# Kernel optimization log

Hardware: AMD Instinct MI355X
Metric: run time of the kernel (lower is better)

## Reference

```python
import jax, jax.numpy as jnp
import numpy as np

EPS = 1e-5  # torch BatchNorm default


def setup_inputs() -> dict:
    key = jax.random.key(0)
    ks = jax.random.split(key, 8)
    B, Q, S, C = 4, 256, 128, 256
    feats = [2 * C, 256, 64, 1]  # opt['num_features']
    inp = {
        "support_features": jax.random.normal(ks[0], (B, S, C), dtype=jnp.float32),
        "query_features": jax.random.normal(ks[1], (B, Q, C), dtype=jnp.float32),
    }
    for i in range(3):
        fan_in, fan_out = feats[i], feats[i + 1]
        std = np.sqrt(2.0 / (fan_in + fan_out))  # xavier_normal on conv weight
        inp[f"W{i}"] = jax.random.normal(ks[2 + i], (fan_out, fan_in), dtype=jnp.float32) * std
        inp[f"b{i}"] = jnp.zeros((fan_out,), dtype=jnp.float32)
        inp[f"g{i}"] = jnp.ones((fan_out,), dtype=jnp.float32)   # BN weight
        inp[f"bt{i}"] = jnp.zeros((fan_out,), dtype=jnp.float32)  # BN bias
    return inp


def _bn_relu(x, g, bt):
    # x: [B, N, C]; BatchNorm1d training-mode stats over batch and length dims
    mean = jnp.mean(x, axis=(0, 1))
    var = jnp.mean(jnp.square(x - mean), axis=(0, 1))  # biased var, as torch BN
    return jax.nn.relu((x - mean) * (g * jax.lax.rsqrt(var + EPS)) + bt)


def reference(support_features, query_features,
              W0, b0, g0, bt0, W1, b1, g1, bt1, W2, b2, g2, bt2):
    B, S, C = support_features.shape
    Q = query_features.shape[1]
    # pairwise concat: [B, Q, S, 2C]
    uq = jnp.broadcast_to(query_features[:, :, None, :], (B, Q, S, C))
    us = jnp.broadcast_to(support_features[:, None, :, :], (B, Q, S, C))
    x = jnp.concatenate([uq, us], axis=3).reshape(B, Q * S, 2 * C)
    # 1x1 conv == matmul over channel dim
    x = _bn_relu(jnp.einsum('bnc,oc->bno', x, W0) + b0, g0, bt0)
    x = _bn_relu(jnp.einsum('bnc,oc->bno', x, W1) + b1, g1, bt1)
    x = _bn_relu(jnp.einsum('bnc,oc->bno', x, W2) + b2, g2, bt2)
    # back to [B, C_out, Q, S]
    return jnp.transpose(x, (0, 2, 1)).reshape(B, -1, Q, S)
```

## Files before the change

### kernel.cpp

```cpp
#include <hip/hip_runtime.h>
#include <hip/hip_bf16.h>


typedef __attribute__((ext_vector_type(4))) float f32x4;
typedef __attribute__((ext_vector_type(8))) short s16x8;

#define BN_EPS 1e-5f
#define INV_N  (1.0f/131072.0f)
#define W1PITCH 264

__device__ __forceinline__ unsigned pk_bf16(float a, float b) {
  float2 t; t.x = a; t.y = b;
  __hip_bfloat162 h = __float22bfloat162_rn(t);
  return *reinterpret_cast<unsigned*>(&h);
}
__device__ __forceinline__ void split2(float a, float b, unsigned& uh, unsigned& ul) {
  uh = pk_bf16(a, b);
  float ha = __uint_as_float(uh << 16);
  float hb = __uint_as_float(uh & 0xFFFF0000u);
  ul = pk_bf16(a - ha, b - hb);
}

union frag_u { s16x8 v; unsigned u[4]; };

struct Args {
  const float *Sf, *Qf, *W0, *b0, *g0, *bt0, *W1, *b1, *g1, *bt1, *W2, *b2, *g2, *bt2;
  float *Aq, *As, *y2, *ws0s, *ws1f, *ws2f, *out;
  ushort *W1h, *W1l;
};

__global__ __launch_bounds__(256) void k_g0(Args a)
{
  int bi = blockIdx.x, t = threadIdx.x;
  if (bi == 96) {
    for (int k = 0; k < 32; k++) {
      int idx = t * 64 + k * 2;
      unsigned uh, ul;
      split2(a.W1[idx], a.W1[idx + 1], uh, ul);
      a.W1h[idx] = (ushort)(uh & 0xFFFFu); a.W1h[idx + 1] = (ushort)(uh >> 16);
      a.W1l[idx] = (ushort)(ul & 0xFFFFu); a.W1l[idx + 1] = (ushort)(ul >> 16);
    }
    for (int i = t; i < 2048; i += 256) a.ws1f[i] = 0.0f;
    if (t < 32) a.ws2f[t] = 0.0f;
    return;
  }
  int w = t >> 6, l = t & 63, l15 = l & 15, quad = l >> 4;
  bool isQ = (bi < 64);
  const float* X; float* Out; int m0, koff;
  if (isQ) { m0 = bi * 16; X = a.Qf; Out = a.Aq; koff = 0; }
  else     { m0 = (bi - 64) * 16; X = a.Sf; Out = a.As; koff = 256; }
  int n0 = w * 64;

  f32x4 acc[4] = {};
#pragma unroll
  for (int ko = 0; ko < 256; ko += 32) {
    const float* row = X + (m0 + l15) * 256 + ko + quad * 8;
    f32x4 v0 = *(const f32x4*)(row);
    f32x4 v1 = *(const f32x4*)(row + 4);
    frag_u ah, al;
#pragma unroll
    for (int j = 0; j < 2; j++) {
      split2(v0[2 * j], v0[2 * j + 1], ah.u[j], al.u[j]);
      split2(v1[2 * j], v1[2 * j + 1], ah.u[2 + j], al.u[2 + j]);
    }
#pragma unroll
    for (int nt = 0; nt < 4; nt++) {
      const float* wrow = a.W0 + (n0 + nt * 16 + l15) * 512 + koff + ko + quad * 8;
      f32x4 w0v = *(const f32x4*)(wrow);
      f32x4 w1v = *(const f32x4*)(wrow + 4);
      frag_u bh, bl;
      split2(w0v[0], w0v[1], bh.u[0], bl.u[0]);
      split2(w0v[2], w0v[3], bh.u[1], bl.u[1]);
      split2(w1v[0], w1v[1], bh.u[2], bl.u[2]);
      split2(w1v[2], w1v[3], bh.u[3], bl.u[3]);
      acc[nt] = __builtin_amdgcn_mfma_f32_16x16x32_bf16(ah.v, bh.v, acc[nt], 0, 0, 0);
      acc[nt] = __builtin_amdgcn_mfma_f32_16x16x32_bf16(al.v, bh.v, acc[nt], 0, 0, 0);
      acc[nt] = __builtin_amdgcn_mfma_f32_16x16x32_bf16(ah.v, bl.v, acc[nt], 0, 0, 0);
    }
  }
#pragma unroll
  for (int nt = 0; nt < 4; nt++) {
    int o = n0 + nt * 16 + l15;
    float bias = isQ ? 0.0f : a.b0[o];
    float cs = 0, cs2 = 0;
#pragma unroll
    for (int r = 0; r < 4; r++) {
      float y = acc[nt][r] + bias;
      Out[(m0 + quad * 4 + r) * 256 + o] = y;
      cs += y; cs2 += y * y;
    }
    cs  += __shfl_xor(cs, 16);  cs  += __shfl_xor(cs, 32);
    cs2 += __shfl_xor(cs2, 16); cs2 += __shfl_xor(cs2, 32);
    if (quad == 0) {
      a.ws0s[bi * 512 + o] = cs;
      a.ws0s[bi * 512 + 256 + o] = cs2;
    }
  }
}

__device__ __forceinline__ void stage_w1(const Args& a, int t, ushort* w1h, ushort* w1l)
{
  int row = t >> 2, qd = t & 3;
  const s16x8* srch = (const s16x8*)(a.W1h + row * 256 + qd * 64);
  const s16x8* srcl = (const s16x8*)(a.W1l + row * 256 + qd * 64);
  s16x8* dsth = (s16x8*)(w1h + row * W1PITCH + qd * 64);
  s16x8* dstl = (s16x8*)(w1l + row * W1PITCH + qd * 64);
#pragma unroll
  for (int k = 0; k < 8; k++) { dsth[k] = srch[k]; dstl[k] = srcl[k]; }
}

__device__ __forceinline__ void mfma_kloop(
    const float* __restrict__ Aq, const float* __restrict__ As,
    const float* sh_a0c0, const ushort* w1h, const ushort* w1l,
    int b, int qt, int st, int w, int l15, int quad, f32x4 acc[4][4])
{
  const float* asrow = As + ((b << 7) + st * 16 + l15) * 256;
  const float* aqrow[4];
#pragma unroll
  for (int mt = 0; mt < 4; mt++)
    aqrow[mt] = Aq + ((b << 8) + qt * 16 + w * 4 + mt) * 256;

#pragma unroll
  for (int ko = 0; ko < 256; ko += 32) {
    int obase = ko + quad * 8;
    f32x4 a0v0 = *(const f32x4*)(sh_a0c0 + obase);
    f32x4 a0v1 = *(const f32x4*)(sh_a0c0 + obase + 4);
    f32x4 c0v0 = *(const f32x4*)(sh_a0c0 + 256 + obase);
    f32x4 c0v1 = *(const f32x4*)(sh_a0c0 + 256 + obase + 4);
    f32x4 as0 = *(const f32x4*)(asrow + obase);
    f32x4 as1 = *(const f32x4*)(asrow + obase + 4);

    s16x8 zh[4];
#pragma unroll
    for (int mt = 0; mt < 4; mt++) {
      f32x4 aq0 = *(const f32x4*)(aqrow[mt] + obase);
      f32x4 aq1 = *(const f32x4*)(aqrow[mt] + obase + 4);
      f32x4 z0 = (aq0 + as0) * a0v0 + c0v0;
      f32x4 z1 = (aq1 + as1) * a0v1 + c0v1;
      frag_u zz;
      zz.u[0] = pk_bf16(fmaxf(z0[0], 0.0f), fmaxf(z0[1], 0.0f));
      zz.u[1] = pk_bf16(fmaxf(z0[2], 0.0f), fmaxf(z0[3], 0.0f));
      zz.u[2] = pk_bf16(fmaxf(z1[0], 0.0f), fmaxf(z1[1], 0.0f));
      zz.u[3] = pk_bf16(fmaxf(z1[2], 0.0f), fmaxf(z1[3], 0.0f));
      zh[mt] = zz.v;
    }
#pragma unroll
    for (int nt = 0; nt < 4; nt++) {
      s16x8 bh = *(const s16x8*)(w1h + (nt * 16 + l15) * W1PITCH + obase);
      s16x8 bl = *(const s16x8*)(w1l + (nt * 16 + l15) * W1PITCH + obase);
#pragma unroll
      for (int mt = 0; mt < 4; mt++) {
        acc[mt][nt] = __builtin_amdgcn_mfma_f32_16x16x32_bf16(zh[mt], bh, acc[mt][nt], 0, 0, 0);
        acc[mt][nt] = __builtin_amdgcn_mfma_f32_16x16x32_bf16(zh[mt], bl, acc[mt][nt], 0, 0, 0);
      }
    }
  }
}

__device__ __forceinline__ void bn0_finalize(const Args& a, int t, float* sh_a0c0)
{
  int o = t;
  float sumY = 0, cross = 0, SQ2 = 0, SS2 = 0;
#pragma unroll
  for (int b = 0; b < 4; b++) {
    float sq1 = 0, sq2 = 0, ss1 = 0, ss2 = 0;
#pragma unroll
    for (int c = 0; c < 16; c++) {
      sq1 += a.ws0s[(b * 16 + c) * 512 + o];
      sq2 += a.ws0s[(b * 16 + c) * 512 + 256 + o];
    }
#pragma unroll
    for (int c = 0; c < 8; c++) {
      ss1 += a.ws0s[(64 + b * 8 + c) * 512 + o];
      ss2 += a.ws0s[(64 + b * 8 + c) * 512 + 256 + o];
    }
    SQ2 += sq2; SS2 += ss2;
    sumY += 128.0f * sq1 + 256.0f * ss1;
    cross += sq1 * ss1;
  }
  float mean = sumY * INV_N;
  float var = (128.0f * SQ2 + 256.0f * SS2 + 2.0f * cross) * INV_N - mean * mean;
  float aa = a.g0[o] * rsqrtf(var + BN_EPS);
  sh_a0c0[o] = aa;
  sh_a0c0[256 + o] = a.bt0[o] - mean * aa;
}

__global__ __launch_bounds__(256) void k_m1(Args a)
{
  int bi = blockIdx.x, t = threadIdx.x;
  int w = t >> 6, l = t & 63, l15 = l & 15, quad = l >> 4;
  __shared__ ushort w1h[64 * W1PITCH];
  __shared__ ushort w1l[64 * W1PITCH];
  __shared__ float sh_a0c0[512];
  __shared__ float red[2][4][4][16];

  stage_w1(a, t, w1h, w1l);
  bn0_finalize(a, t, sh_a0c0);
  __syncthreads();

  int b_ = bi >> 7, rem = bi & 127, qt = rem >> 3, st = rem & 7;
  f32x4 acc[4][4] = {};
  mfma_kloop(a.Aq, a.As, sh_a0c0, w1h, w1l, b_, qt, st, w, l15, quad, acc);

#pragma unroll
  for (int nt = 0; nt < 4; nt++) {
    float bias = a.b1[nt * 16 + l15];
    float s = 0, s2 = 0;
#pragma unroll
    for (int mt = 0; mt < 4; mt++)
#pragma unroll
      for (int r = 0; r < 4; r++) {
        float y = acc[mt][nt][r] + bias;
        s += y; s2 += y * y;
      }
    s  += __shfl_xor(s, 16);  s  += __shfl_xor(s, 32);
    s2 += __shfl_xor(s2, 16); s2 += __shfl_xor(s2, 32);
    if (quad == 0) { red[0][w][nt][l15] = s; red[1][w][nt][l15] = s2; }
  }
  __syncthreads();
  if (t < 128) {
    int which = t >> 6, j = t & 63, nt = j >> 4, jl = j & 15;
    float v = red[which][0][nt][jl] + red[which][1][nt][jl] +
              red[which][2][nt][jl] + red[which][3][nt][jl];
    atomicAdd(&a.ws1f[(bi & 15) * 128 + t], v);
  }
}

__global__ __launch_bounds__(256) void k_m2(Args a)
{
  int bi = blockIdx.x, t = threadIdx.x;
  int w = t >> 6, l = t & 63, l15 = l & 15, quad = l >> 4;
  __shared__ ushort w1h[64 * W1PITCH];
  __shared__ ushort w1l[64 * W1PITCH];
  __shared__ float sh_a0c0[512];
  __shared__ float sh_tot[128];
  __shared__ float sh_a1c1[128];
  __shared__ float rs[16], rs2[16];

  stage_w1(a, t, w1h, w1l);
  bn0_finalize(a, t, sh_a0c0);
  if (t < 128) {
    float accv = 0;
#pragma unroll
    for (int c = 0; c < 16; c++) accv += a.ws1f[c * 128 + t];
    sh_tot[t] = accv;
  }
  __syncthreads();
  if (t < 64) {
    float mean = sh_tot[t] * INV_N;
    float var = sh_tot[64 + t] * INV_N - mean * mean;
    float aa = a.g1[t] * rsqrtf(var + BN_EPS);
    sh_a1c1[t] = aa;
    sh_a1c1[64 + t] = a.bt1[t] - mean * aa;
  }
  __syncthreads();

  int b_ = bi >> 7, rem = bi & 127, qt = rem >> 3, st = rem & 7;
  f32x4 acc[4][4] = {};
  mfma_kloop(a.Aq, a.As, sh_a0c0, w1h, w1l, b_, qt, st, w, l15, quad, acc);

  float a1v[4], c1v[4], w2v[4], biasv[4];
#pragma unroll
  for (int nt = 0; nt < 4; nt++) {
    int j = nt * 16 + l15;
    a1v[nt] = sh_a1c1[j]; c1v[nt] = sh_a1c1[64 + j];
    w2v[nt] = a.W2[j]; biasv[nt] = a.b1[j];
  }
  float b2v = a.b2[0];
  float ls = 0, ls2 = 0;
#pragma unroll
  for (int mt = 0; mt < 4; mt++) {
    float part[4] = {0, 0, 0, 0};
#pragma unroll
    for (int nt = 0; nt < 4; nt++)
#pragma unroll
      for (int r = 0; r < 4; r++) {
        float y = acc[mt][nt][r] + biasv[nt];
        float z = fmaxf(a1v[nt] * y + c1v[nt], 0.0f);
        part[r] += z * w2v[nt];
      }
#pragma unroll
    for (int r = 0; r < 4; r++) {
      float p = part[r];
      p += __shfl_xor(p, 1); p += __shfl_xor(p, 2);
      p += __shfl_xor(p, 4); p += __shfl_xor(p, 8);
      part[r] = p + b2v;
    }
    if (l15 == 0) {
      int q = qt * 16 + w * 4 + mt;
      int P = ((b_ * 256 + q) * 128) + st * 16 + quad * 4;
      f32x4 o;
#pragma unroll
      for (int r = 0; r < 4; r++) { o[r] = part[r]; ls += part[r]; ls2 += part[r] * part[r]; }
      *(f32x4*)(a.y2 + P) = o;
    }
  }
  if (l15 == 0) { rs[t >> 4] = ls; rs2[t >> 4] = ls2; }
  __syncthreads();
  if (t == 0) {
    float s = 0, s2 = 0;
#pragma unroll
    for (int i = 0; i < 16; i++) { s += rs[i]; s2 += rs2[i]; }
    atomicAdd(&a.ws2f[(bi & 15) * 2], s);
    atomicAdd(&a.ws2f[(bi & 15) * 2 + 1], s2);
  }
}

__global__ __launch_bounds__(256) void k_out(Args a)
{
  int t = threadIdx.x;
  float s = 0, s2 = 0;
#pragma unroll
  for (int c = 0; c < 16; c++) { s += a.ws2f[c * 2]; s2 += a.ws2f[c * 2 + 1]; }
  float mean = s * INV_N;
  float var = s2 * INV_N - mean * mean;
  float aa = a.g2[0] * rsqrtf(var + BN_EPS);
  float cc = a.bt2[0] - mean * aa;
  int i = (blockIdx.x * 256 + t) * 4;
  f32x4 v = *(const f32x4*)(a.y2 + i);
  f32x4 o;
#pragma unroll
  for (int r = 0; r < 4; r++) o[r] = fmaxf(aa * v[r] + cc, 0.0f);
  *(f32x4*)(a.out + i) = o;
}

extern "C" void kernel_launch(void* const* d_in, const int* in_sizes, int n_in,
                              void* d_out, int out_size, void* d_ws, size_t ws_size,
                              hipStream_t stream)
{
  float* ws = (float*)d_ws;
  Args a;
  a.Sf  = (const float*)d_in[0];
  a.Qf  = (const float*)d_in[1];
  a.W0  = (const float*)d_in[2];
  a.b0  = (const float*)d_in[3];
  a.g0  = (const float*)d_in[4];
  a.bt0 = (const float*)d_in[5];
  a.W1  = (const float*)d_in[6];
  a.b1  = (const float*)d_in[7];
  a.g1  = (const float*)d_in[8];
  a.bt1 = (const float*)d_in[9];
  a.W2  = (const float*)d_in[10];
  a.b2  = (const float*)d_in[11];
  a.g2  = (const float*)d_in[12];
  a.bt2 = (const float*)d_in[13];

  a.Aq   = ws;
  a.As   = ws + 262144;
  a.y2   = ws + 393216;
  a.ws0s = ws + 524288;
  a.ws1f = ws + 573440;
  a.ws2f = ws + 575488;
  a.W1h  = (ushort*)(ws + 575552);
  a.W1l  = (ushort*)(ws + 583744);
  a.out  = (float*)d_out;

  k_g0 <<<97, 256, 0, stream>>>(a);
  k_m1 <<<512, 256, 0, stream>>>(a);
  k_m2 <<<512, 256, 0, stream>>>(a);
  k_out<<<128, 256, 0, stream>>>(a);
}
```

Baseline: 144.2 us.

## Materialize layer-1 output in bf16 instead of recomputing GEMM in second pass

```diff
diff --git a/kernel.cpp b/kernel.cpp
--- a/kernel.cpp
+++ b/kernel.cpp
@@ -7,7 +7,6 @@
 
 #define BN_EPS 1e-5f
 #define INV_N  (1.0f/131072.0f)
-#define W1PITCH 264
 
 __device__ __forceinline__ unsigned pk_bf16(float a, float b) {
   float2 t; t.x = a; t.y = b;
@@ -26,7 +25,7 @@
 struct Args {
   const float *Sf, *Qf, *W0, *b0, *g0, *bt0, *W1, *b1, *g1, *bt1, *W2, *b2, *g2, *bt2;
   float *Aq, *As, *y2, *ws0s, *ws1f, *ws2f, *out;
-  ushort *W1h, *W1l;
+  ushort *W1h, *W1l, *y1f;
 };
 
 __global__ __launch_bounds__(256) void k_g0(Args a)
@@ -98,31 +97,65 @@
   }
 }
 
-__device__ __forceinline__ void stage_w1(const Args& a, int t, ushort* w1h, ushort* w1l)
-{
-  int row = t >> 2, qd = t & 3;
-  const s16x8* srch = (const s16x8*)(a.W1h + row * 256 + qd * 64);
-  const s16x8* srcl = (const s16x8*)(a.W1l + row * 256 + qd * 64);
-  s16x8* dsth = (s16x8*)(w1h + row * W1PITCH + qd * 64);
-  s16x8* dstl = (s16x8*)(w1l + row * W1PITCH + qd * 64);
-#pragma unroll
-  for (int k = 0; k < 8; k++) { dsth[k] = srch[k]; dstl[k] = srcl[k]; }
-}
-
-__device__ __forceinline__ void mfma_kloop(
-    const float* __restrict__ Aq, const float* __restrict__ As,
-    const float* sh_a0c0, const ushort* w1h, const ushort* w1l,
-    int b, int qt, int st, int w, int l15, int quad, f32x4 acc[4][4])
-{
-  const float* asrow = As + ((b << 7) + st * 16 + l15) * 256;
+__device__ __forceinline__ void bn0_finalize(const Args& a, int t, float* sh_a0c0)
+{
+  int o = t;
+  float sumY = 0, cross = 0, SQ2 = 0, SS2 = 0;
+#pragma unroll
+  for (int b = 0; b < 4; b++) {
+    float sq1 = 0, sq2 = 0, ss1 = 0, ss2 = 0;
+#pragma unroll
+    for (int c = 0; c < 16; c++) {
+      sq1 += a.ws0s[(b * 16 + c) * 512 + o];
+      sq2 += a.ws0s[(b * 16 + c) * 512 + 256 + o];
+    }
+#pragma unroll
+    for (int c = 0; c < 8; c++) {
+      ss1 += a.ws0s[(64 + b * 8 + c) * 512 + o];
+      ss2 += a.ws0s[(64 + b * 8 + c) * 512 + 256 + o];
+    }
+    SQ2 += sq2; SS2 += ss2;
+    sumY += 128.0f * sq1 + 256.0f * ss1;
+    cross += sq1 * ss1;
+  }
+  float mean = sumY * INV_N;
+  float var = (128.0f * SQ2 + 256.0f * SS2 + 2.0f * cross) * INV_N - mean * mean;
+  float aa = a.g0[o] * rsqrtf(var + BN_EPS);
+  sh_a0c0[o] = aa;
+  sh_a0c0[256 + o] = a.bt0[o] - mean * aa;
+}
+
+__global__ __launch_bounds__(256) void k_m1(Args a)
+{
+  int bi = blockIdx.x, t = threadIdx.x;
+  int w = t >> 6, l = t & 63, l15 = l & 15, quad = l >> 4;
+  __shared__ ushort w1hf[2048 * 8];
+  __shared__ ushort w1lf[2048 * 8];
+  __shared__ float sh_a0c0[512];
+  __shared__ float red[2][4][4][16];
+
+#pragma unroll
+  for (int i = 0; i < 8; i++) {
+    int fr = i * 256 + t;
+    int kk = fr >> 8, r = fr & 255, nt = r >> 6, ln = r & 63;
+    int src = (nt * 16 + (ln & 15)) * 256 + kk * 32 + (ln >> 4) * 8;
+    *(s16x8*)(w1hf + fr * 8) = *(const s16x8*)(a.W1h + src);
+    *(s16x8*)(w1lf + fr * 8) = *(const s16x8*)(a.W1l + src);
+  }
+  bn0_finalize(a, t, sh_a0c0);
+  __syncthreads();
+
+  int b_ = bi >> 7, rem = bi & 127, qt = rem >> 3, st = rem & 7;
+  const float* asrow = a.As + ((b_ << 7) + st * 16 + l15) * 256;
   const float* aqrow[4];
 #pragma unroll
   for (int mt = 0; mt < 4; mt++)
-    aqrow[mt] = Aq + ((b << 8) + qt * 16 + w * 4 + mt) * 256;
-
-#pragma unroll
-  for (int ko = 0; ko < 256; ko += 32) {
-    int obase = ko + quad * 8;
+    aqrow[mt] = a.Aq + ((b_ << 8) + qt * 16 + w * 4 + mt) * 256;
+
+  f32x4 acc[4][4] = {};
+#pragma unroll
+  for (int kk = 0; kk < 8; kk++) {
+    int obase = kk * 32 + quad * 8;
     f32x4 a0v0 = *(const f32x4*)(sh_a0c0 + obase);
     f32x4 a0v1 = *(const f32x4*)(sh_a0c0 + obase + 4);
     f32x4 c0v0 = *(const f32x4*)(sh_a0c0 + 256 + obase);
@@ -146,8 +179,8 @@
     }
 #pragma unroll
     for (int nt = 0; nt < 4; nt++) {
-      s16x8 bh = *(const s16x8*)(w1h + (nt * 16 + l15) * W1PITCH + obase);
-      s16x8 bl = *(const s16x8*)(w1l + (nt * 16 + l15) * W1PITCH + obase);
+      s16x8 bh = *(const s16x8*)(w1hf + ((kk * 4 + nt) * 64 + l) * 8);
+      s16x8 bl = *(const s16x8*)(w1lf + ((kk * 4 + nt) * 64 + l) * 8);
 #pragma unroll
       for (int mt = 0; mt < 4; mt++) {
         acc[mt][nt] = __builtin_amdgcn_mfma_f32_16x16x32_bf16(zh[mt], bh, acc[mt][nt], 0, 0, 0);
@@ -155,67 +188,35 @@
       }
     }
   }
-}
-
-__device__ __forceinline__ void bn0_finalize(const Args& a, int t, float* sh_a0c0)
-{
-  int o = t;
-  float sumY = 0, cross = 0, SQ2 = 0, SS2 = 0;
-#pragma unroll
-  for (int b = 0; b < 4; b++) {
-    float sq1 = 0, sq2 = 0, ss1 = 0, ss2 = 0;
-#pragma unroll
-    for (int c = 0; c < 16; c++) {
-      sq1 += a.ws0s[(b * 16 + c) * 512 + o];
-      sq2 += a.ws0s[(b * 16 + c) * 512 + 256 + o];
-    }
-#pragma unroll
-    for (int c = 0; c < 8; c++) {
-      ss1 += a.ws0s[(64 + b * 8 + c) * 512 + o];
-      ss2 += a.ws0s[(64 + b * 8 + c) * 512 + 256 + o];
-    }
-    SQ2 += sq2; SS2 += ss2;
-    sumY += 128.0f * sq1 + 256.0f * ss1;
-    cross += sq1 * ss1;
-  }
-  float mean = sumY * INV_N;
-  float var = (128.0f * SQ2 + 256.0f * SS2 + 2.0f * cross) * INV_N - mean * mean;
-  float aa = a.g0[o] * rsqrtf(var + BN_EPS);
-  sh_a0c0[o] = aa;
-  sh_a0c0[256 + o] = a.bt0[o] - mean * aa;
-}
-
-__global__ __launch_bounds__(256) void k_m1(Args a)
-{
-  int bi = blockIdx.x, t = threadIdx.x;
-  int w = t >> 6, l = t & 63, l15 = l & 15, quad = l >> 4;
-  __shared__ ushort w1h[64 * W1PITCH];
-  __shared__ ushort w1l[64 * W1PITCH];
-  __shared__ float sh_a0c0[512];
-  __shared__ float red[2][4][4][16];
-
-  stage_w1(a, t, w1h, w1l);
-  bn0_finalize(a, t, sh_a0c0);
-  __syncthreads();
-
-  int b_ = bi >> 7, rem = bi & 127, qt = rem >> 3, st = rem & 7;
-  f32x4 acc[4][4] = {};
-  mfma_kloop(a.Aq, a.As, sh_a0c0, w1h, w1l, b_, qt, st, w, l15, quad, acc);
-
+
+  float biasv[4];
+#pragma unroll
+  for (int nt = 0; nt < 4; nt++) biasv[nt] = a.b1[nt * 16 + l15];
+  float s[4] = {0, 0, 0, 0}, s2[4] = {0, 0, 0, 0};
+#pragma unroll
+  for (int mt = 0; mt < 4; mt++) {
+#pragma unroll
+    for (int nt = 0; nt < 4; nt++) {
+      float y0 = acc[mt][nt][0] + biasv[nt];
+      float y1 = acc[mt][nt][1] + biasv[nt];
+      float y2v = acc[mt][nt][2] + biasv[nt];
+      float y3 = acc[mt][nt][3] + biasv[nt];
+      unsigned u01 = pk_bf16(y0, y1), u23 = pk_bf16(y2v, y3);
+      uint2 pk; pk.x = u01; pk.y = u23;
+      int slot = (bi * 4 + w) * 16 + mt * 4 + nt;
+      *(uint2*)(a.y1f + (size_t)(slot * 64 + l) * 4) = pk;
+      float f0 = __uint_as_float(u01 << 16), f1 = __uint_as_float(u01 & 0xFFFF0000u);
+      float f2 = __uint_as_float(u23 << 16), f3 = __uint_as_float(u23 & 0xFFFF0000u);
+      s[nt]  += f0 + f1 + f2 + f3;
+      s2[nt] += f0 * f0 + f1 * f1 + f2 * f2 + f3 * f3;
+    }
+  }
 #pragma unroll
   for (int nt = 0; nt < 4; nt++) {
-    float bias = a.b1[nt * 16 + l15];
-    float s = 0, s2 = 0;
-#pragma unroll
-    for (int mt = 0; mt < 4; mt++)
-#pragma unroll
-      for (int r = 0; r < 4; r++) {
-        float y = acc[mt][nt][r] + bias;
-        s += y; s2 += y * y;
-      }
-    s  += __shfl_xor(s, 16);  s  += __shfl_xor(s, 32);
-    s2 += __shfl_xor(s2, 16); s2 += __shfl_xor(s2, 32);
-    if (quad == 0) { red[0][w][nt][l15] = s; red[1][w][nt][l15] = s2; }
+    float v = s[nt], v2 = s2[nt];
+    v  += __shfl_xor(v, 16);  v  += __shfl_xor(v, 32);
+    v2 += __shfl_xor(v2, 16); v2 += __shfl_xor(v2, 32);
+    if (quad == 0) { red[0][w][nt][l15] = v; red[1][w][nt][l15] = v2; }
   }
   __syncthreads();
   if (t < 128) {
@@ -226,19 +227,14 @@
   }
 }
 
-__global__ __launch_bounds__(256) void k_m2(Args a)
-{
-  int bi = blockIdx.x, t = threadIdx.x;
+__global__ __launch_bounds__(256) void k_p2(Args a)
+{
+  int p = blockIdx.x, t = threadIdx.x;
   int w = t >> 6, l = t & 63, l15 = l & 15, quad = l >> 4;
-  __shared__ ushort w1h[64 * W1PITCH];
-  __shared__ ushort w1l[64 * W1PITCH];
-  __shared__ float sh_a0c0[512];
   __shared__ float sh_tot[128];
   __shared__ float sh_a1c1[128];
   __shared__ float rs[16], rs2[16];
 
-  stage_w1(a, t, w1h, w1l);
-  bn0_finalize(a, t, sh_a0c0);
   if (t < 128) {
     float accv = 0;
 #pragma unroll
@@ -255,54 +251,59 @@
   }
   __syncthreads();
 
-  int b_ = bi >> 7, rem = bi & 127, qt = rem >> 3, st = rem & 7;
-  f32x4 acc[4][4] = {};
-  mfma_kloop(a.Aq, a.As, sh_a0c0, w1h, w1l, b_, qt, st, w, l15, quad, acc);
-
-  float a1v[4], c1v[4], w2v[4], biasv[4];
+  float a1v[4], c1v[4], w2v[4];
 #pragma unroll
   for (int nt = 0; nt < 4; nt++) {
     int j = nt * 16 + l15;
-    a1v[nt] = sh_a1c1[j]; c1v[nt] = sh_a1c1[64 + j];
-    w2v[nt] = a.W2[j]; biasv[nt] = a.b1[j];
+    a1v[nt] = sh_a1c1[j]; c1v[nt] = sh_a1c1[64 + j]; w2v[nt] = a.W2[j];
   }
   float b2v = a.b2[0];
   float ls = 0, ls2 = 0;
-#pragma unroll
-  for (int mt = 0; mt < 4; mt++) {
-    float part[4] = {0, 0, 0, 0};
-#pragma unroll
-    for (int nt = 0; nt < 4; nt++)
+
+#pragma unroll
+  for (int task = 0; task < 2; task++) {
+    int gw = (p * 4 + w) * 2 + task;
+    int bi = gw >> 2, w1 = gw & 3;
+    int b = bi >> 7, rem = bi & 127, qt = rem >> 3, st = rem & 7;
+#pragma unroll
+    for (int mt = 0; mt < 4; mt++) {
+      float part[4] = {0, 0, 0, 0};
+#pragma unroll
+      for (int nt = 0; nt < 4; nt++) {
+        int slot = (bi * 4 + w1) * 16 + mt * 4 + nt;
+        uint2 v = *(const uint2*)(a.y1f + (size_t)(slot * 64 + l) * 4);
+        float f0 = __uint_as_float(v.x << 16), f1 = __uint_as_float(v.x & 0xFFFF0000u);
+        float f2 = __uint_as_float(v.y << 16), f3 = __uint_as_float(v.y & 0xFFFF0000u);
+        part[0] += fmaxf(a1v[nt] * f0 + c1v[nt], 0.0f) * w2v[nt];
+        part[1] += fmaxf(a1v[nt] * f1 + c1v[nt], 0.0f) * w2v[nt];
+        part[2] += fmaxf(a1v[nt] * f2 + c1v[nt], 0.0f) * w2v[nt];
+        part[3] += fmaxf(a1v[nt] * f3 + c1v[nt], 0.0f) * w2v[nt];
+      }
 #pragma unroll
       for (int r = 0; r < 4; r++) {
-        float y = acc[mt][nt][r] + biasv[nt];
-        float z = fmaxf(a1v[nt] * y + c1v[nt], 0.0f);
-        part[r] += z * w2v[nt];
+        float pv = part[r];
+        pv += __shfl_xor(pv, 1); pv += __shfl_xor(pv, 2);
+        pv += __shfl_xor(pv, 4); pv += __shfl_xor(pv, 8);
+        part[r] = pv + b2v;
       }
-#pragma unroll
-    for (int r = 0; r < 4; r++) {
-      float p = part[r];
-      p += __shfl_xor(p, 1); p += __shfl_xor(p, 2);
-      p += __shfl_xor(p, 4); p += __shfl_xor(p, 8);
-      part[r] = p + b2v;
-    }
-    if (l15 == 0) {
-      int q = qt * 16 + w * 4 + mt;
-      int P = ((b_ * 256 + q) * 128) + st * 16 + quad * 4;
-      f32x4 o;
-#pragma unroll
-      for (int r = 0; r < 4; r++) { o[r] = part[r]; ls += part[r]; ls2 += part[r] * part[r]; }
-      *(f32x4*)(a.y2 + P) = o;
+      if (l15 == 0) {
+        int q = qt * 16 + w1 * 4 + mt;
+        int P = ((b * 256 + q) * 128) + st * 16 + quad * 4;
+        f32x4 o;
+#pragma unroll
+        for (int r = 0; r < 4; r++) { o[r] = part[r]; ls += part[r]; ls2 += part[r] * part[r]; }
+        *(f32x4*)(a.y2 + P) = o;
+      }
     }
   }
   if (l15 == 0) { rs[t >> 4] = ls; rs2[t >> 4] = ls2; }
   __syncthreads();
   if (t == 0) {
-    float s = 0, s2 = 0;
-#pragma unroll
-    for (int i = 0; i < 16; i++) { s += rs[i]; s2 += rs2[i]; }
-    atomicAdd(&a.ws2f[(bi & 15) * 2], s);
-    atomicAdd(&a.ws2f[(bi & 15) * 2 + 1], s2);
+    float sv = 0, sv2 = 0;
+#pragma unroll
+    for (int i = 0; i < 16; i++) { sv += rs[i]; sv2 += rs2[i]; }
+    atomicAdd(&a.ws2f[(p & 15) * 2], sv);
+    atomicAdd(&a.ws2f[(p & 15) * 2 + 1], sv2);
   }
 }
 
@@ -353,10 +354,11 @@
   a.ws2f = ws + 575488;
   a.W1h  = (ushort*)(ws + 575552);
   a.W1l  = (ushort*)(ws + 583744);
+  a.y1f  = (ushort*)(ws + 591936);
   a.out  = (float*)d_out;
 
   k_g0 <<<97, 256, 0, stream>>>(a);
   k_m1 <<<512, 256, 0, stream>>>(a);
-  k_m2 <<<512, 256, 0, stream>>>(a);
+  k_p2 <<<256, 256, 0, stream>>>(a);
   k_out<<<128, 256, 0, stream>>>(a);
 }
```

After: 137.6 us. 4.6% less time.
